# Kernel tuning notes

Measured on AMD Instinct MI355X. Metric: run time of the kernel, lower is better.

The kernel has to match this reference:

```python
import jax, jax.numpy as jnp
import numpy as np

B, T, S, D, H, FF = 4, 1024, 1024, 1024, 16, 4096
DH = D // H
NEG = -1e9
EPS = 1e-5


def setup_inputs() -> dict:
    key = jax.random.key(0)
    ks = jax.random.split(key, 20)
    p = 0.02  # param init scale
    inp = {
        "x": jax.random.normal(ks[0], (B, T, D), jnp.float32),
        "encoder_output": jax.random.normal(ks[1], (B, S, D), jnp.float32),
        "src_mask": jnp.ones((B, 1, 1, S), jnp.bool_),
        "tgt_mask": jnp.tril(jnp.ones((1, 1, T, T), jnp.bool_)),  # causal
        # self-attention params
        "d_Wq": jax.random.normal(ks[2], (D, D)) * p, "d_bq": jnp.zeros((D,)),
        "d_Wk": jax.random.normal(ks[3], (D, D)) * p, "d_bk": jnp.zeros((D,)),
        "d_Wv": jax.random.normal(ks[4], (D, D)) * p, "d_bv": jnp.zeros((D,)),
        "d_Wo": jax.random.normal(ks[5], (D, D)) * p, "d_bo": jnp.zeros((D,)),
        # cross-attention params
        "e_Wq": jax.random.normal(ks[6], (D, D)) * p, "e_bq": jnp.zeros((D,)),
        "e_Wk": jax.random.normal(ks[7], (D, D)) * p, "e_bk": jnp.zeros((D,)),
        "e_Wv": jax.random.normal(ks[8], (D, D)) * p, "e_bv": jnp.zeros((D,)),
        "e_Wo": jax.random.normal(ks[9], (D, D)) * p, "e_bo": jnp.zeros((D,)),
        # FFN params
        "ff_W1": jax.random.normal(ks[10], (D, FF)) * p, "ff_b1": jnp.zeros((FF,)),
        "ff_W2": jax.random.normal(ks[11], (FF, D)) * p, "ff_b2": jnp.zeros((D,)),
        # layernorm params
        "ln1_g": jnp.ones((D,)), "ln1_b": jnp.zeros((D,)),
        "ln2_g": jnp.ones((D,)), "ln2_b": jnp.zeros((D,)),
        "ln3_g": jnp.ones((D,)), "ln3_b": jnp.zeros((D,)),
    }
    return inp


def _mha(xq, xkv, Wq, bq, Wk, bk, Wv, bv, Wo, bo, mask):
    b, tq = xq.shape[0], xq.shape[1]
    q = (xq @ Wq + bq).reshape(b, tq, H, DH).transpose(0, 2, 1, 3)
    k = (xkv @ Wk + bk).reshape(b, -1, H, DH).transpose(0, 2, 1, 3)
    v = (xkv @ Wv + bv).reshape(b, -1, H, DH).transpose(0, 2, 1, 3)
    scores = jnp.einsum("bhqd,bhkd->bhqk", q, k) / np.float32(np.sqrt(DH))
    scores = jnp.where(mask, scores, NEG)
    attn = jax.nn.softmax(scores, axis=-1)
    out = jnp.einsum("bhqk,bhkd->bhqd", attn, v)
    out = out.transpose(0, 2, 1, 3).reshape(b, tq, D)
    return out @ Wo + bo


def _ln(x, g, b):
    m = jnp.mean(x, axis=-1, keepdims=True)
    v = jnp.var(x, axis=-1, keepdims=True)
    return (x - m) / jnp.sqrt(v + EPS) * g + b


def reference(x, encoder_output, src_mask, tgt_mask,
              d_Wq, d_bq, d_Wk, d_bk, d_Wv, d_bv, d_Wo, d_bo,
              e_Wq, e_bq, e_Wk, e_bk, e_Wv, e_bv, e_Wo, e_bo,
              ff_W1, ff_b1, ff_W2, ff_b2,
              ln1_g, ln1_b, ln2_g, ln2_b, ln3_g, ln3_b):
    # masked self-attention + residual + LN (dropout is identity in eval)
    d = _mha(x, x, d_Wq, d_bq, d_Wk, d_bk, d_Wv, d_bv, d_Wo, d_bo, tgt_mask)
    d = _ln(d + x, ln1_g, ln1_b)
    # cross-attention over encoder output + residual + LN
    f = _mha(d, encoder_output, e_Wq, e_bq, e_Wk, e_bk, e_Wv, e_bv, e_Wo, e_bo, src_mask)
    f = _ln(f + d, ln2_g, ln2_b)
    # FFN + residual + LN
    g = jax.nn.relu(f @ ff_W1 + ff_b1) @ ff_W2 + ff_b2
    g = _ln(g + f, ln3_g, ln3_b)
    return g
```

## Files before the change

kernel.cpp:

```cpp
#include <hip/hip_runtime.h>

static constexpr int Bc = 4, Tc = 1024, Sc = 1024, Dc = 1024, Hc = 16, DHc = 64, FFc = 4096;

typedef __attribute__((ext_vector_type(8))) short short8;
typedef __attribute__((ext_vector_type(4))) short short4v;
typedef __attribute__((ext_vector_type(4))) float f32x4;

struct P8 { unsigned short* o[8]; };

__device__ __forceinline__ unsigned short f2bf(float f) {
    unsigned int u = __float_as_uint(f);
    unsigned int r = u + 0x7fffu + ((u >> 16) & 1u);
    return (unsigned short)(r >> 16);
}
__device__ __forceinline__ float bf2f(unsigned short u) {
    return __uint_as_float(((unsigned int)u) << 16);
}
__device__ __forceinline__ float fexp2(float x) {
    float r; asm("v_exp_f32 %0, %1" : "=v"(r) : "v"(x)); return r;
}
__device__ __forceinline__ unsigned int cvtpk(float a, float b) {
    unsigned int r;
    asm("v_cvt_pk_bf16_f32 %0, %1, %2" : "=v"(r) : "v"(a), "v"(b));
    return r;
}

__device__ __forceinline__ void gload_lds16(const void* g, void* l) {
    __builtin_amdgcn_global_load_lds((const __attribute__((address_space(1))) void*)g,
                                     (__attribute__((address_space(3))) void*)l, 16, 0, 0);
}

__global__ __launch_bounds__(256) void cast2_f32_bf16(const float* __restrict__ inA,
                                                      const float* __restrict__ inB,
                                                      unsigned short* __restrict__ outA,
                                                      unsigned short* __restrict__ outB, int n8) {
    int i = blockIdx.x * 256 + threadIdx.x;
    if (i >= n8) return;
    const float* in = blockIdx.y ? inB : inA;
    unsigned short* out = blockIdx.y ? outB : outA;
    const float4* p = (const float4*)in + (size_t)i * 2;
    float4 a = p[0], b = p[1];
    short8 o;
    o[0] = f2bf(a.x); o[1] = f2bf(a.y); o[2] = f2bf(a.z); o[3] = f2bf(a.w);
    o[4] = f2bf(b.x); o[5] = f2bf(b.y); o[6] = f2bf(b.z); o[7] = f2bf(b.w);
    *(short8*)(out + (size_t)i * 8) = o;
}

struct TJ { const float* s; unsigned short* d; int ss, ds; float scl; };
struct TJ16 { TJ j[16]; };
__global__ __launch_bounds__(256) void transpose_cast16(TJ16 p) {
    __shared__ float t[64][65];
    const TJ jb = p.j[blockIdx.z];
    const int c0 = blockIdx.x * 64, r0 = blockIdx.y * 64;
    const int tid = threadIdx.x;
    const int rr = tid >> 2, cc = (tid & 3) * 16;
    const float* src = jb.s + (size_t)(r0 + rr) * jb.ss + c0 + cc;
#pragma unroll
    for (int i = 0; i < 4; i++) {
        float4 v = *(const float4*)(src + i * 4);
        t[rr][cc + i * 4 + 0] = v.x;
        t[rr][cc + i * 4 + 1] = v.y;
        t[rr][cc + i * 4 + 2] = v.z;
        t[rr][cc + i * 4 + 3] = v.w;
    }
    __syncthreads();
#pragma unroll
    for (int half = 0; half < 2; half++) {
        const int id = half * 256 + tid;
        const int a = id >> 3, b0 = id & 7;
        short8 o;
#pragma unroll
        for (int e = 0; e < 8; e++) o[e] = f2bf(t[b0 * 8 + e][a] * jb.scl);
        *(short8*)(jb.d + (size_t)(c0 + a) * jb.ds + r0 + b0 * 8) = o;
    }
}

__global__ void prep_bias(const float* dbq, const float* dbk, const float* dbv,
                          const float* ebk, const float* ebv, const float* ebq,
                          float* __restrict__ bqkv, float* __restrict__ bekv,
                          float* __restrict__ ebq_s, float SC) {
    int i = blockIdx.x * 256 + threadIdx.x;
    int seg = i >> 10, j = i & 1023;
    switch (seg) {
        case 0: bqkv[j] = dbq[j] * SC; break;
        case 1: bqkv[1024 + j] = dbk[j]; break;
        case 2: bqkv[2048 + j] = dbv[j]; break;
        case 3: bekv[j] = ebk[j]; break;
        case 4: bekv[1024 + j] = ebv[j]; break;
        default: ebq_s[j] = ebq[j] * SC; break;
    }
}

struct BlkMap { int m, n, z; };
__device__ __forceinline__ BlkMap remap_block() {
    const int gx = gridDim.x, gy = gridDim.y;
    const int nxy = gx * gy;
    const int nwg = nxy * gridDim.z;
    const int flat = (blockIdx.z * gy + blockIdx.y) * gx + blockIdx.x;
    const int id = (flat & 7) * (nwg >> 3) + (flat >> 3);
    const int pz = id / nxy;
    const int rz = id - pz * nxy;
    const int gwsh = (gx & 7) ? 2 : 3;
    const int gw = 1 << gwsh;
    const int gsz = gw * gy;
    const int grp = rz / gsz;
    const int rem = rz - grp * gsz;
    BlkMap r;
    r.m = rem >> gwsh;
    r.n = (grp << gwsh) + (rem & (gw - 1));
    r.z = pz;
    return r;
}

#define G256_BODY()                                                                            \
    stB(0, 0, 0); stA(0, 0, 0); stB(0, 1, 0); stA(0, 1, 0);                                    \
    stB(1, 0, 64); stA(1, 0, 64); stB(1, 1, 64);                                               \
    asm volatile("s_waitcnt vmcnt(6)" ::: "memory");                                           \
    __builtin_amdgcn_s_barrier();                                                              \
    const int nIter = nk >> 1;                                                                 \
    for (int it = 0; it < nIter; ++it) {                                                       \
        const int t_ = 2 * it, u_ = t_ + 1;                                                    \
        const int ku = u_ * 64;                                                                \
        const int kv = ((t_ + 2 < nk) ? t_ + 2 : t_) * 64;                                     \
        const int kw = ((u_ + 2 < nk) ? u_ + 2 : u_) * 64;                                     \
        ldB(0, 0, b0); ldA(0, 0, aF, aH);                                                      \
        stA(1, 1, ku);                                                                         \
        asm volatile("s_waitcnt lgkmcnt(8)" ::: "memory");                                     \
        __builtin_amdgcn_s_barrier();                                                          \
        asm volatile("s_waitcnt lgkmcnt(0)" ::: "memory");                                     \
        __builtin_amdgcn_s_setprio(1); MFMA16(aF, b0, 0); __builtin_amdgcn_s_setprio(0);       \
        __builtin_amdgcn_s_barrier();                                                          \
        ldB(0, 1, b1);                                                                         \
        stB(0, 0, kv);                                                                         \
        __builtin_amdgcn_s_barrier();                                                          \
        asm volatile("s_waitcnt lgkmcnt(0)" ::: "memory");                                     \
        __builtin_amdgcn_s_setprio(1); MFMA16(aH, b1, 0); __builtin_amdgcn_s_setprio(0);       \
        __builtin_amdgcn_s_barrier();                                                          \
        ldA(0, 1, aF, aH);                                                                     \
        stA(0, 0, kv);                                                                         \
        __builtin_amdgcn_s_barrier();                                                          \
        asm volatile("s_waitcnt lgkmcnt(0)" ::: "memory");                                     \
        __builtin_amdgcn_s_setprio(1); MFMA16(aH, b1, 4); __builtin_amdgcn_s_setprio(0);       \
        __builtin_amdgcn_s_barrier();                                                          \
        stB(0, 1, kv);                                                                         \
        __builtin_amdgcn_s_barrier();                                                          \
        __builtin_amdgcn_s_setprio(1); MFMA16(aF, b0, 4); __builtin_amdgcn_s_setprio(0);       \
        asm volatile("s_waitcnt vmcnt(6)" ::: "memory");                                       \
        __builtin_amdgcn_s_barrier();                                                          \
        ldB(1, 0, b0); ldA(1, 0, aF, aH);                                                      \
        stA(0, 1, kv);                                                                         \
        asm volatile("s_waitcnt lgkmcnt(8)" ::: "memory");                                     \
        __builtin_amdgcn_s_barrier();                                                          \
        asm volatile("s_waitcnt lgkmcnt(0)" ::: "memory");                                     \
        __builtin_amdgcn_s_setprio(1); MFMA16(aF, b0, 0); __builtin_amdgcn_s_setprio(0);       \
        __builtin_amdgcn_s_barrier();                                                          \
        ldB(1, 1, b1);                                                                         \
        stB(1, 0, kw);                                                                         \
        __builtin_amdgcn_s_barrier();                                                          \
        asm volatile("s_waitcnt lgkmcnt(0)" ::: "memory");                                     \
        __builtin_amdgcn_s_setprio(1); MFMA16(aH, b1, 0); __builtin_amdgcn_s_setprio(0);       \
        __builtin_amdgcn_s_barrier();                                                          \
        ldA(1, 1, aF, aH);                                                                     \
        stA(1, 0, kw);                                                                         \
        __builtin_amdgcn_s_barrier();                                                          \
        asm volatile("s_waitcnt lgkmcnt(0)" ::: "memory");                                     \
        __builtin_amdgcn_s_setprio(1); MFMA16(aH, b1, 4); __builtin_amdgcn_s_setprio(0);       \
        __builtin_amdgcn_s_barrier();                                                          \
        stB(1, 1, kw);                                                                         \
        __builtin_amdgcn_s_barrier();                                                          \
        __builtin_amdgcn_s_setprio(1); MFMA16(aF, b0, 4); __builtin_amdgcn_s_setprio(0);       \
        asm volatile("s_waitcnt vmcnt(6)" ::: "memory");                                       \
        __builtin_amdgcn_s_barrier();                                                          \
    }                                                                                          \
    asm volatile("s_waitcnt vmcnt(0)" ::: "memory");                                           \
    __syncthreads();

#define MFMA16(aa, bb, base)                                                                   \
    _Pragma("unroll") for (int m_ = 0; m_ < 4; m_++)                                           \
        _Pragma("unroll") for (int n_ = 0; n_ < 4; n_++)                                       \
            acc[(base) + m_][n_] = __builtin_amdgcn_mfma_f32_16x16x32_bf16(                    \
                (aa)[m_], (bb)[n_], acc[(base) + m_][n_], 0, 0, 0);

template <int EPI>
__global__ __launch_bounds__(512, 2) void gemm256(const unsigned short* __restrict__ A,
                                                  const unsigned short* __restrict__ Bt,
                                                  const float* __restrict__ bias,
                                                  unsigned short* __restrict__ outB,
                                                  int N, int lda, int ldb, int nk, P8 po) {
    __shared__ unsigned short SM[2][2][2][8192];
    const int tid = threadIdx.x;
    const int lane = tid & 63, wid = tid >> 6;
    const int l4 = lane & 15, g = lane >> 4;
    const int wr = wid >> 2, wc = wid & 3;
    BlkMap bm = remap_block();
    const int m0 = bm.m * 256, n0 = bm.n * 256, z = bm.z;
    A += (size_t)z * (nk * 64);
    Bt += (size_t)z * (nk * 64);
    const int sw = l4 & 7;

    const int fl0 = tid, fl1 = 512 + tid;
    const int lr0 = fl0 >> 3, ch0 = (fl0 & 7) ^ (lr0 & 7);
    const int lr1 = fl1 >> 3, ch1 = (fl1 & 7) ^ (lr1 & 7);
    const size_t A64 = (size_t)64 * lda;
    const unsigned short* pA0 = A + (size_t)(m0 + (lr0 >> 6) * 128 + (lr0 & 63)) * lda + ch0 * 8;
    const unsigned short* pA1 = A + (size_t)(m0 + (lr1 >> 6) * 128 + (lr1 & 63)) * lda + ch1 * 8;
    const unsigned short* pB0 = Bt + (size_t)(n0 + (ch0 >> 2) * 128 + lr0) * ldb + (ch0 & 3) * 8;
    const unsigned short* pB1 = Bt + (size_t)(n0 + (ch1 >> 2) * 128 + lr1) * ldb + (ch1 & 3) * 8;

    auto stA = [&](int d, int mh, int kofs) {
        char* base = (char*)&SM[0][d][mh][0];
        gload_lds16(pA0 + (size_t)mh * A64 + kofs, base + fl0 * 16);
        gload_lds16(pA1 + (size_t)mh * A64 + kofs, base + fl1 * 16);
    };
    auto stB = [&](int d, int ks, int kofs) {
        char* base = (char*)&SM[1][d][ks][0];
        gload_lds16(pB0 + ks * 32 + kofs, base + fl0 * 16);
        gload_lds16(pB1 + ks * 32 + kofs, base + fl1 * 16);
    };

    f32x4 acc[8][4] = {};
    short8 aF[4], aH[4], b0[4], b1[4];

    auto ldA = [&](int d, int mh, short8* d0, short8* d1) {
#pragma unroll
        for (int m = 0; m < 4; m++) {
            const char* rp = (const char*)&SM[0][d][mh][0] + (wr * 64 + m * 16 + l4) * 128;
            d0[m] = *(const short8*)(rp + ((g ^ sw) * 16));
            d1[m] = *(const short8*)(rp + (((4 + g) ^ sw) * 16));
        }
    };
    auto ldB = [&](int d, int ks, short8* dst) {
#pragma unroll
        for (int n = 0; n < 4; n++) {
            const char* rp = (const char*)&SM[1][d][ks][0] + ((wc & 1) * 64 + n * 16 + l4) * 128;
            dst[n] = *(const short8*)(rp + ((((wc >> 1) * 4 + g) ^ sw) * 16));
        }
    };

    G256_BODY()

    unsigned short* eb = (unsigned short*)SM;
    unsigned short* oB = (EPI == 3) ? po.o[z] : outB;
    const int colL = wc * 64 + l4;
#pragma unroll
    for (int h = 0; h < 2; ++h) {
        if (wr == h) {
#pragma unroll
            for (int mm = 0; mm < 8; mm++) {
                const int base_r = (mm < 4 ? mm * 16 : 64 + (mm - 4) * 16) + g * 4;
#pragma unroll
                for (int n = 0; n < 4; n++) {
                    float bv = (EPI == 3 && z != 0) ? 0.f : bias[n0 + colL + n * 16];
#pragma unroll
                    for (int r = 0; r < 4; r++) {
                        float v = acc[mm][n][r] + bv;
                        if (EPI == 2) v = fmaxf(v, 0.f);
                        eb[(base_r + r) * 260 + colL + n * 16] = f2bf(v);
                    }
                }
            }
        }
        __syncthreads();
        const int gr0 = m0 + h * 128;
#pragma unroll
        for (int j = 0; j < 8; j++) {
            const int f = j * 8192 + tid * 16;
            const int row = f >> 9;
            const int colb = f & 511;
            short8 v = *(const short8*)((const char*)eb + row * 520 + colb);
            *(short8*)(oB + (size_t)(gr0 + row) * N + n0 + (colb >> 1)) = v;
        }
        if (h == 0) __syncthreads();
    }
}

struct GJob {
    const unsigned short *A, *Bt;
    const float* bias;
    unsigned short *out, *vt;
    int N, lda, ldb, nk, vthresh, nwg, gx;
};
struct GJ2 { GJob j[2]; };
__global__ __launch_bounds__(512, 2) void gemm256j(GJ2 p) {
    __shared__ unsigned short SM[2][2][2][8192];
    const int tid = threadIdx.x;
    const int lane = tid & 63, wid = tid >> 6;
    const int l4 = lane & 15, g = lane >> 4;
    const int wr = wid >> 2, wc = wid & 3;

    int f = blockIdx.x;
    const int ji = (f < p.j[0].nwg) ? 0 : 1;
    if (ji) f -= p.j[0].nwg;
    const GJob jb = p.j[ji];
    const int id = (f & 7) * (jb.nwg >> 3) + (f >> 3);
    const int gwsh = (jb.gx & 7) ? 2 : 3;
    const int gw = 1 << gwsh;
    const int gy = jb.nwg / jb.gx;
    const int gsz = gw * gy;
    const int grp = id / gsz;
    const int rem = id - grp * gsz;
    const int m0 = (rem >> gwsh) * 256;
    const int n0 = ((grp << gwsh) + (rem & (gw - 1))) * 256;

    const unsigned short* A = jb.A;
    const unsigned short* Bt = jb.Bt;
    const int lda = jb.lda, ldb = jb.ldb, nk = jb.nk;
    const int sw = l4 & 7;

    const int fl0 = tid, fl1 = 512 + tid;
    const int lr0 = fl0 >> 3, ch0 = (fl0 & 7) ^ (lr0 & 7);
    const int lr1 = fl1 >> 3, ch1 = (fl1 & 7) ^ (lr1 & 7);
    const size_t A64 = (size_t)64 * lda;
    const unsigned short* pA0 = A + (size_t)(m0 + (lr0 >> 6) * 128 + (lr0 & 63)) * lda + ch0 * 8;
    const unsigned short* pA1 = A + (size_t)(m0 + (lr1 >> 6) * 128 + (lr1 & 63)) * lda + ch1 * 8;
    const unsigned short* pB0 = Bt + (size_t)(n0 + (ch0 >> 2) * 128 + lr0) * ldb + (ch0 & 3) * 8;
    const unsigned short* pB1 = Bt + (size_t)(n0 + (ch1 >> 2) * 128 + lr1) * ldb + (ch1 & 3) * 8;

    auto stA = [&](int d, int mh, int kofs) {
        char* base = (char*)&SM[0][d][mh][0];
        gload_lds16(pA0 + (size_t)mh * A64 + kofs, base + fl0 * 16);
        gload_lds16(pA1 + (size_t)mh * A64 + kofs, base + fl1 * 16);
    };
    auto stB = [&](int d, int ks, int kofs) {
        char* base = (char*)&SM[1][d][ks][0];
        gload_lds16(pB0 + ks * 32 + kofs, base + fl0 * 16);
        gload_lds16(pB1 + ks * 32 + kofs, base + fl1 * 16);
    };

    f32x4 acc[8][4] = {};
    short8 aF[4], aH[4], b0[4], b1[4];

    auto ldA = [&](int d, int mh, short8* d0, short8* d1) {
#pragma unroll
        for (int m = 0; m < 4; m++) {
            const char* rp = (const char*)&SM[0][d][mh][0] + (wr * 64 + m * 16 + l4) * 128;
            d0[m] = *(const short8*)(rp + ((g ^ sw) * 16));
            d1[m] = *(const short8*)(rp + (((4 + g) ^ sw) * 16));
        }
    };
    auto ldB = [&](int d, int ks, short8* dst) {
#pragma unroll
        for (int n = 0; n < 4; n++) {
            const char* rp = (const char*)&SM[1][d][ks][0] + ((wc & 1) * 64 + n * 16 + l4) * 128;
            dst[n] = *(const short8*)(rp + ((((wc >> 1) * 4 + g) ^ sw) * 16));
        }
    };

    G256_BODY()

    unsigned short* eb = (unsigned short*)SM;
    const int colL = wc * 64 + l4;
#pragma unroll
    for (int h = 0; h < 2; ++h) {
        if (wr == h) {
#pragma unroll
            for (int mm = 0; mm < 8; mm++) {
                const int base_r = (mm < 4 ? mm * 16 : 64 + (mm - 4) * 16) + g * 4;
#pragma unroll
                for (int n = 0; n < 4; n++) {
                    float bv = jb.bias[n0 + colL + n * 16];
#pragma unroll
                    for (int r = 0; r < 4; r++)
                        eb[(base_r + r) * 260 + colL + n * 16] = f2bf(acc[mm][n][r] + bv);
                }
            }
        }
        __syncthreads();
        const int gr0 = m0 + h * 128;
        if (n0 >= jb.vthresh) {
            const int b_ = gr0 >> 10, sb = gr0 & 1023;
#pragma unroll
            for (int j = 0; j < 4; j++) {
                const int id2 = j * 512 + tid;
                const int col = id2 & 255, rseg = id2 >> 8;
                const int rel = n0 - jb.vthresh + col;
                const int hh = rel >> 6, dh = rel & 63;
                short8 v0, v1;
#pragma unroll
                for (int e = 0; e < 8; e++) {
                    v0[e] = eb[(rseg * 16 + e) * 260 + col];
                    v1[e] = eb[(rseg * 16 + 8 + e) * 260 + col];
                }
                unsigned short* dp = jb.vt +
                    ((size_t)(b_ * 16 + hh) * 64 + dh) * 1024 + sb + rseg * 16;
                *(short8*)dp = v0;
                *(short8*)(dp + 8) = v1;
            }
        } else {
#pragma unroll
            for (int j = 0; j < 8; j++) {
                const int ff = j * 8192 + tid * 16;
                const int row = ff >> 9;
                const int colb = ff & 511;
                short8 v = *(const short8*)((const char*)eb + row * 520 + colb);
                *(short8*)(jb.out + (size_t)(gr0 + row) * jb.N + n0 + (colb >> 1)) = v;
            }
        }
        if (h == 0) __syncthreads();
    }
}

template <int EPI>
__global__ __launch_bounds__(256) void gemm64_db(const unsigned short* __restrict__ A,
                                                 const unsigned short* __restrict__ Bt,
                                                 const float* __restrict__ bias,
                                                 float* __restrict__ outF,
                                                 unsigned short* __restrict__ outB,
                                                 int M, int N, int Kloop, int lda, int ldb) {
    __shared__ unsigned short As[3][64 * 32];
    __shared__ unsigned short Bs[3][128 * 32];
    const int tid = threadIdx.x;
    const int w = tid >> 6, lane = tid & 63, l4 = lane & 15, g = lane >> 4;
    BlkMap bm = remap_block();
    const int m0 = bm.m * 64, n0 = bm.n * 128;
    f32x4 acc[4][2] = {};
    const int r0 = tid >> 2;
    const int kk = ((tid & 3) ^ ((tid >> 3) & 3)) * 8;
    const int sk = (l4 >> 1) & 3;
    const unsigned short* Ar0 = A + (size_t)(m0 + r0) * lda + kk;
    const unsigned short* Br0 = Bt + (size_t)(n0 + r0) * ldb + kk;
    const unsigned short* Br1 = Bt + (size_t)(n0 + 64 + r0) * ldb + kk;
    auto stage = [&](int sb, int k0) {
        gload_lds16(Ar0 + k0, (char*)As[sb] + tid * 16);
        gload_lds16(Br0 + k0, (char*)Bs[sb] + tid * 16);
        gload_lds16(Br1 + k0, (char*)Bs[sb] + 4096 + tid * 16);
    };
    const int nk = Kloop >> 5;
    stage(0, 0);
    stage(1, 32);
    asm volatile("s_waitcnt vmcnt(3)" ::: "memory");
    __builtin_amdgcn_s_barrier();
    asm volatile("" ::: "memory");
    int buf = 0;
    for (int t = 0; t < nk; ++t) {
        if (t + 2 < nk) {
            int b2 = buf + 2; if (b2 >= 3) b2 -= 3;
            stage(b2, (t + 2) * 32);
        }
        short8 a[4], b[2];
#pragma unroll
        for (int m = 0; m < 4; m++)
            a[m] = *(const short8*)(As[buf] + (m * 16 + l4) * 32 + (g ^ sk) * 8);
#pragma unroll
        for (int n = 0; n < 2; n++)
            b[n] = *(const short8*)(Bs[buf] + (w * 32 + n * 16 + l4) * 32 + (g ^ sk) * 8);
#pragma unroll
        for (int m = 0; m < 4; m++)
#pragma unroll
            for (int n = 0; n < 2; n++)
                acc[m][n] = __builtin_amdgcn_mfma_f32_16x16x32_bf16(a[m], b[n], acc[m][n], 0, 0, 0);
        if (t + 1 < nk) {
            if (t + 2 < nk) asm volatile("s_waitcnt vmcnt(3)" ::: "memory");
            else            asm volatile("s_waitcnt vmcnt(0)" ::: "memory");
            __builtin_amdgcn_s_barrier();
            asm volatile("" ::: "memory");
        }
        buf = (buf + 1 == 3) ? 0 : buf + 1;
    }
    const int rowB = m0 + g * 4;
    const int colB = n0 + w * 32 + l4;
#pragma unroll
    for (int n = 0; n < 2; n++) {
        float bv = bias[colB + n * 16];
#pragma unroll
        for (int m = 0; m < 4; m++) {
#pragma unroll
            for (int r = 0; r < 4; r++) {
                float v = acc[m][n][r] + bv;
                if (EPI == 2) v = fmaxf(v, 0.f);
                size_t idx = (size_t)(rowB + m * 16 + r) * N + colB + n * 16;
                if (EPI == 1) outF[idx] = v;
                else outB[idx] = f2bf(v);
            }
        }
    }
}

template <int CAUSAL>
__global__ __launch_bounds__(512) void attn6_kernel(const unsigned short* __restrict__ Q, int ldq,
                                                    const unsigned short* __restrict__ Kg, int ldk,
                                                    const unsigned short* __restrict__ Vt,
                                                    unsigned short* __restrict__ O) {
    __shared__ unsigned short Kl[2 * 64 * 64];
    __shared__ unsigned short Vl[2 * 64 * 64];
    __shared__ unsigned short Pl[8][16 * 72];
    const int bh = blockIdx.x;
    const int qb = CAUSAL ? (gridDim.y - 1 - blockIdx.y) : blockIdx.y;
    const int b = bh >> 4, h = bh & 15;
    const int tid = threadIdx.x, w = tid >> 6, lane = tid & 63;
    const int l4 = lane & 15, g = lane >> 4;
    const int q0 = qb * 128 + w * 16;
    const unsigned short* Qp = Q + (size_t)(b * Tc + q0 + l4) * ldq + h * DHc + g * 8;
    short8 qf0 = *(const short8*)Qp;
    short8 qf1 = *(const short8*)(Qp + 32);
    const unsigned short* Kbase = Kg + (size_t)(b * 1024) * ldk + h * DHc;
    const unsigned short* Vbase = Vt + (size_t)bh * DHc * 1024;
    f32x4 o[4] = {};
    float mrun = -1e30f, lrun = 0.f;
    const int nT = CAUSAL ? 2 * qb + 2 : 16;
    unsigned short* pw = &Pl[w][l4 * 72];
    const int qi = q0 + l4;

    short8 ones;
#pragma unroll
    for (int j = 0; j < 8; j++) ones[j] = (short)0x3F80;

    const int sr = tid >> 3;
    const int sc_ = (tid & 7) ^ (sr & 7);

    auto stage = [&](int s0, int buf) {
        char* kd = (char*)Kl + buf * 8192;
        char* vd = (char*)Vl + buf * 8192;
        gload_lds16(Kbase + (size_t)(s0 + sr) * ldk + sc_ * 8, kd + tid * 16);
        gload_lds16(Vbase + (size_t)sr * 1024 + s0 + sc_ * 8, vd + tid * 16);
    };

    stage(0, 0);
    __syncthreads();
    int buf = 0;
    const int sw = l4 & 7;

    for (int t = 0; t < nT; ++t) {
        const int s0 = t * 64;
        if (t + 1 < nT) stage(s0 + 64, buf ^ 1);
        if (!CAUSAL || s0 <= q0 + 15) {
            const unsigned short* Kb_ = Kl + buf * 4096;
            const unsigned short* Vb_ = Vl + buf * 4096;
            f32x4 st[4];
            f32x4 z = {0.f, 0.f, 0.f, 0.f};
            __builtin_amdgcn_s_setprio(1);
#pragma unroll
            for (int c = 0; c < 4; c++) {
                const unsigned short* kr = Kb_ + (c * 16 + l4) * 64;
                short8 ka0 = *(const short8*)(kr + ((g ^ sw) * 8));
                short8 ka1 = *(const short8*)(kr + (((g + 4) ^ sw) * 8));
                st[c] = __builtin_amdgcn_mfma_f32_16x16x32_bf16(ka0, qf0, z, 0, 0, 0);
                st[c] = __builtin_amdgcn_mfma_f32_16x16x32_bf16(ka1, qf1, st[c], 0, 0, 0);
            }
            __builtin_amdgcn_s_setprio(0);
            float p[16];
            const bool domask = CAUSAL && (s0 + 63 > q0);
#pragma unroll
            for (int c = 0; c < 4; c++)
#pragma unroll
                for (int r = 0; r < 4; r++) {
                    float v = st[c][r];
                    if (domask && (s0 + c * 16 + g * 4 + r) > qi) v = -1e9f;
                    p[c * 4 + r] = v;
                }
            float m1 = fmaxf(fmaxf(p[0], p[1]), p[2]);
            float m2 = fmaxf(fmaxf(p[3], p[4]), p[5]);
            float m3 = fmaxf(fmaxf(p[6], p[7]), p[8]);
            float m4 = fmaxf(fmaxf(p[9], p[10]), p[11]);
            float m5 = fmaxf(fmaxf(p[12], p[13]), p[14]);
            float tmax = fmaxf(fmaxf(fmaxf(m1, m2), fmaxf(m3, m4)), fmaxf(m5, p[15]));
            tmax = fmaxf(tmax, __shfl_xor(tmax, 16));
            tmax = fmaxf(tmax, __shfl_xor(tmax, 32));
            if (!__all(tmax <= mrun + 11.5f)) {
                float mnew = fmaxf(mrun, tmax);
                float al = fexp2(mrun - mnew);
                lrun *= al;
#pragma unroll
                for (int d = 0; d < 4; d++) o[d] *= al;
                mrun = mnew;
            }
#pragma unroll
            for (int i = 0; i < 16; i++) p[i] = fexp2(p[i] - mrun);
#pragma unroll
            for (int c = 0; c < 4; c++) {
                uint2 u;
                u.x = cvtpk(p[c * 4 + 0], p[c * 4 + 1]);
                u.y = cvtpk(p[c * 4 + 2], p[c * 4 + 3]);
                *(uint2*)(pw + c * 16 + g * 4) = u;
            }
            short8 pb_lo = *(const short8*)(pw + g * 8);
            short8 pb_hi = *(const short8*)(pw + 32 + g * 8);
            __builtin_amdgcn_s_setprio(1);
            f32x4 s4 = __builtin_amdgcn_mfma_f32_16x16x32_bf16(ones, pb_lo, z, 0, 0, 0);
            s4 = __builtin_amdgcn_mfma_f32_16x16x32_bf16(ones, pb_hi, s4, 0, 0, 0);
#pragma unroll
            for (int d = 0; d < 4; d++) {
                const unsigned short* vr = Vb_ + (d * 16 + l4) * 64;
                short8 va0 = *(const short8*)(vr + ((g ^ sw) * 8));
                short8 va1 = *(const short8*)(vr + (((g + 4) ^ sw) * 8));
                o[d] = __builtin_amdgcn_mfma_f32_16x16x32_bf16(va0, pb_lo, o[d], 0, 0, 0);
                o[d] = __builtin_amdgcn_mfma_f32_16x16x32_bf16(va1, pb_hi, o[d], 0, 0, 0);
            }
            __builtin_amdgcn_s_setprio(0);
            lrun += s4[0];
        }
        __syncthreads();
        buf ^= 1;
    }
    float inv = 1.f / lrun;
    unsigned short* Ob = O + (size_t)(b * Tc + q0 + l4) * Dc + h * DHc;
#pragma unroll
    for (int d = 0; d < 4; d++) {
#pragma unroll
        for (int r = 0; r < 4; r++) Ob[d * 16 + g * 4 + r] = f2bf(o[d][r] * inv);
    }
}

__global__ __launch_bounds__(256) void ln_bf(const unsigned short* __restrict__ a,
                                             const unsigned short* __restrict__ res,
                                             const float* __restrict__ gam,
                                             const float* __restrict__ bet,
                                             unsigned short* __restrict__ outB,
                                             float* __restrict__ outF) {
    int row = blockIdx.x, t = threadIdx.x;
    size_t base = (size_t)row * Dc + t * 4;
    short4v av = *(const short4v*)(a + base);
    short4v rv = *(const short4v*)(res + base);
    float x0 = bf2f((unsigned short)av[0]) + bf2f((unsigned short)rv[0]);
    float x1 = bf2f((unsigned short)av[1]) + bf2f((unsigned short)rv[1]);
    float x2 = bf2f((unsigned short)av[2]) + bf2f((unsigned short)rv[2]);
    float x3 = bf2f((unsigned short)av[3]) + bf2f((unsigned short)rv[3]);
    float s = x0 + x1 + x2 + x3;
    float ss = x0 * x0 + x1 * x1 + x2 * x2 + x3 * x3;
    for (int o = 1; o < 64; o <<= 1) { s += __shfl_xor(s, o); ss += __shfl_xor(ss, o); }
    __shared__ float S1[4], S2[4];
    int w = t >> 6;
    if ((t & 63) == 0) { S1[w] = s; S2[w] = ss; }
    __syncthreads();
    s = S1[0] + S1[1] + S1[2] + S1[3];
    ss = S2[0] + S2[1] + S2[2] + S2[3];
    float mean = s * (1.f / Dc);
    float var = ss * (1.f / Dc) - mean * mean;
    float rstd = rsqrtf(var + 1e-5f);
    int c = t * 4;
    float4 g4 = *(const float4*)(gam + c);
    float4 b4 = *(const float4*)(bet + c);
    float y0 = (x0 - mean) * rstd * g4.x + b4.x;
    float y1 = (x1 - mean) * rstd * g4.y + b4.y;
    float y2 = (x2 - mean) * rstd * g4.z + b4.z;
    float y3 = (x3 - mean) * rstd * g4.w + b4.w;
    if (outB) {
        short4v ob;
        ob[0] = f2bf(y0); ob[1] = f2bf(y1); ob[2] = f2bf(y2); ob[3] = f2bf(y3);
        *(short4v*)(outB + base) = ob;
    }
    if (outF) { float4 ov = {y0, y1, y2, y3}; *(float4*)(outF + base) = ov; }
}

__global__ __launch_bounds__(256) void ln_4b(const unsigned short* __restrict__ p,
                                             const unsigned short* __restrict__ res,
                                             const float* __restrict__ gam,
                                             const float* __restrict__ bet,
                                             float* __restrict__ outF) {
    const size_t PS = (size_t)4096 * 1024;
    int row = blockIdx.x, t = threadIdx.x;
    size_t base = (size_t)row * Dc + t * 4;
    float x0, x1, x2, x3;
    {
        short4v rv = *(const short4v*)(res + base);
        x0 = bf2f((unsigned short)rv[0]); x1 = bf2f((unsigned short)rv[1]);
        x2 = bf2f((unsigned short)rv[2]); x3 = bf2f((unsigned short)rv[3]);
    }
#pragma unroll
    for (int j = 0; j < 4; j++) {
        short4v v = *(const short4v*)(p + j * PS + base);
        x0 += bf2f((unsigned short)v[0]); x1 += bf2f((unsigned short)v[1]);
        x2 += bf2f((unsigned short)v[2]); x3 += bf2f((unsigned short)v[3]);
    }
    float s = x0 + x1 + x2 + x3;
    float ss = x0 * x0 + x1 * x1 + x2 * x2 + x3 * x3;
    for (int o = 1; o < 64; o <<= 1) { s += __shfl_xor(s, o); ss += __shfl_xor(ss, o); }
    __shared__ float S1[4], S2[4];
    int w = t >> 6;
    if ((t & 63) == 0) { S1[w] = s; S2[w] = ss; }
    __syncthreads();
    s = S1[0] + S1[1] + S1[2] + S1[3];
    ss = S2[0] + S2[1] + S2[2] + S2[3];
    float mean = s * (1.f / Dc);
    float var = ss * (1.f / Dc) - mean * mean;
    float rstd = rsqrtf(var + 1e-5f);
    int c = t * 4;
    float4 g4 = *(const float4*)(gam + c);
    float4 b4 = *(const float4*)(bet + c);
    float4 ov;
    ov.x = (x0 - mean) * rstd * g4.x + b4.x;
    ov.y = (x1 - mean) * rstd * g4.y + b4.y;
    ov.z = (x2 - mean) * rstd * g4.z + b4.z;
    ov.w = (x3 - mean) * rstd * g4.w + b4.w;
    *(float4*)(outF + base) = ov;
}

extern "C" void kernel_launch(void* const* d_in, const int* in_sizes, int n_in,
                              void* d_out, int out_size, void* d_ws, size_t ws_size,
                              hipStream_t stream) {
    const float* x   = (const float*)d_in[0];
    const float* enc = (const float*)d_in[1];
    const float* dWq = (const float*)d_in[4];  const float* dbq = (const float*)d_in[5];
    const float* dWk = (const float*)d_in[6];  const float* dbk = (const float*)d_in[7];
    const float* dWv = (const float*)d_in[8];  const float* dbv = (const float*)d_in[9];
    const float* dWo = (const float*)d_in[10]; const float* dbo = (const float*)d_in[11];
    const float* eWq = (const float*)d_in[12]; const float* ebq = (const float*)d_in[13];
    const float* eWk = (const float*)d_in[14]; const float* ebk = (const float*)d_in[15];
    const float* eWv = (const float*)d_in[16]; const float* ebv = (const float*)d_in[17];
    const float* eWo = (const float*)d_in[18]; const float* ebo = (const float*)d_in[19];
    const float* fW1 = (const float*)d_in[20]; const float* fb1 = (const float*)d_in[21];
    const float* fW2 = (const float*)d_in[22]; const float* fb2 = (const float*)d_in[23];
    const float* g1 = (const float*)d_in[24];  const float* be1 = (const float*)d_in[25];
    const float* g2 = (const float*)d_in[26];  const float* be2 = (const float*)d_in[27];
    const float* g3 = (const float*)d_in[28];  const float* be3 = (const float*)d_in[29];

    const float SC = 0.125f * 1.44269504f;

    char* ws = (char*)d_ws;
    size_t off = 0;
    auto alloc = [&](size_t bytes) -> void* {
        void* p = ws + off;
        off += (bytes + 255) & ~(size_t)255;
        return p;
    };
    const size_t A = (size_t)4096 * 1024;
    const size_t MB1 = (size_t)1024 * 1024;
    char* R1 = (char*)alloc(32 * 1024 * 1024);
    unsigned short* qkv = (unsigned short*)R1;
    unsigned short* qx  = (unsigned short*)(R1 + 16 * 1024 * 1024);
    unsigned short* h1  = (unsigned short*)R1;
    unsigned short* xb   = (unsigned short*)alloc(A * 2);
    unsigned short* encb = (unsigned short*)alloc(A * 2);
    unsigned short* wqkv = (unsigned short*)alloc(3 * MB1 * 2);
    unsigned short* wekv = (unsigned short*)alloc(2 * MB1 * 2);
    unsigned short* weq  = (unsigned short*)alloc(MB1 * 2);
    unsigned short* wdo  = (unsigned short*)alloc(MB1 * 2);
    unsigned short* weo  = (unsigned short*)alloc(MB1 * 2);
    unsigned short* wf1  = (unsigned short*)alloc(4 * MB1 * 2);
    unsigned short* wf2  = (unsigned short*)alloc(4 * MB1 * 2);
    float* bqkv = (float*)alloc(3072 * 4);
    float* bekv = (float*)alloc(2048 * 4);
    float* ebq_s = (float*)alloc(1024 * 4);
    unsigned short* VtB = (unsigned short*)alloc(A * 2);
    unsigned short* ab  = (unsigned short*)alloc(A * 2);
    unsigned short* tmpB = (unsigned short*)alloc(A * 2);
    unsigned short* dB = (unsigned short*)alloc(A * 2);
    unsigned short* fB = (unsigned short*)alloc(A * 2);
    unsigned short* kb  = (unsigned short*)alloc(A * 2);
    unsigned short* vtc = (unsigned short*)alloc(A * 2);
    unsigned short* pfb = VtB;
    (void)ws_size; (void)in_sizes; (void)n_in; (void)out_size;

    cast2_f32_bf16<<<dim3(2048, 2), 256, 0, stream>>>(x, enc, xb, encb, (int)(A / 8));

    TJ16 tj;
    tj.j[0] = {dWq, wqkv,           1024, 1024, SC};
    tj.j[1] = {dWk, wqkv + MB1,     1024, 1024, 1.f};
    tj.j[2] = {dWv, wqkv + 2 * MB1, 1024, 1024, 1.f};
    tj.j[3] = {eWk, wekv,           1024, 1024, 1.f};
    tj.j[4] = {eWv, wekv + MB1,     1024, 1024, 1.f};
    tj.j[5] = {eWq, weq,            1024, 1024, SC};
    tj.j[6] = {dWo, wdo,            1024, 1024, 1.f};
    tj.j[7] = {eWo, weo,            1024, 1024, 1.f};
    for (int jj = 0; jj < 4; jj++) {
        tj.j[8 + jj]  = {fW1 + 1024 * jj, wf1 + (size_t)1024 * jj * 1024, 4096, 1024, 1.f};
        tj.j[12 + jj] = {fW2 + (size_t)1024 * jj * 1024, wf2 + 1024 * jj, 1024, 4096, 1.f};
    }
    transpose_cast16<<<dim3(16, 16, 16), 256, 0, stream>>>(tj);
    prep_bias<<<24, 256, 0, stream>>>(dbq, dbk, dbv, ebk, ebv, ebq, bqkv, bekv, ebq_s, SC);

    P8 z8{};

    {
        GJ2 gj;
        gj.j[0] = {xb, wqkv, bqkv, qkv, VtB, 3072, 1024, 1024, 16, 2048, 192, 12};
        gj.j[1] = {encb, wekv, bekv, kb, vtc, 1024, 1024, 1024, 16, 1024, 128, 8};
        gemm256j<<<dim3(320), 512, 0, stream>>>(gj);
    }

    attn6_kernel<1><<<dim3(64, 8), 512, 0, stream>>>(qkv, 3072, qkv + 1024, 3072, VtB, ab);
    gemm64_db<0><<<dim3(8, 64), 256, 0, stream>>>(ab, wdo, dbo, nullptr, tmpB, 4096, 1024, 1024, 1024, 1024);
    ln_bf<<<4096, 256, 0, stream>>>(tmpB, xb, g1, be1, dB, nullptr);

    gemm64_db<0><<<dim3(8, 64), 256, 0, stream>>>(dB, weq, ebq_s, nullptr, qx, 4096, 1024, 1024, 1024, 1024);
    attn6_kernel<0><<<dim3(64, 8), 512, 0, stream>>>(qx, 1024, kb, 1024, vtc, ab);
    gemm64_db<0><<<dim3(8, 64), 256, 0, stream>>>(ab, weo, ebo, nullptr, tmpB, 4096, 1024, 1024, 1024, 1024);
    ln_bf<<<4096, 256, 0, stream>>>(tmpB, dB, g2, be2, fB, nullptr);

    gemm256<2><<<dim3(16, 16), 512, 0, stream>>>(fB, wf1, fb1, h1, 4096, 1024, 1024, 16, z8);
    {
        P8 pf{};
        pf.o[0] = pfb;
        pf.o[1] = pfb + A;
        pf.o[2] = pfb + 2 * A;
        pf.o[3] = pfb + 3 * A;
        gemm256<3><<<dim3(4, 16, 4), 512, 0, stream>>>(h1, wf2, fb2, nullptr, 1024, 4096, 4096, 16, pf);
    }
    ln_4b<<<4096, 256, 0, stream>>>(pfb, fB, g3, be3, (float*)d_out);
}
```

Before: 313.8 us.

## Replace 256x256 FFN GEMM with 128x256 tile kernel and simpler double buffering

Swaps the 256x256-tile gemm256 kernel used for both FFN GEMMs for a new 128x256-tile kernel with K-step 32 and a plain two-stage LDS double buffer, launched with 4 blocks per CU. This doubles the block count (512 instead of 256 for FF1) to improve CU occupancy and wave balance on the many-CU device. The cost is lower arithmetic intensity per tile, more global reloads of the B operand, and more barrier iterations per K.

```diff
diff --git a/kernel.cpp b/kernel.cpp
--- a/kernel.cpp
+++ b/kernel.cpp
@@ -181,99 +181,6 @@
             acc[(base) + m_][n_] = __builtin_amdgcn_mfma_f32_16x16x32_bf16(                    \
                 (aa)[m_], (bb)[n_], acc[(base) + m_][n_], 0, 0, 0);
 
-template <int EPI>
-__global__ __launch_bounds__(512, 2) void gemm256(const unsigned short* __restrict__ A,
-                                                  const unsigned short* __restrict__ Bt,
-                                                  const float* __restrict__ bias,
-                                                  unsigned short* __restrict__ outB,
-                                                  int N, int lda, int ldb, int nk, P8 po) {
-    __shared__ unsigned short SM[2][2][2][8192];
-    const int tid = threadIdx.x;
-    const int lane = tid & 63, wid = tid >> 6;
-    const int l4 = lane & 15, g = lane >> 4;
-    const int wr = wid >> 2, wc = wid & 3;
-    BlkMap bm = remap_block();
-    const int m0 = bm.m * 256, n0 = bm.n * 256, z = bm.z;
-    A += (size_t)z * (nk * 64);
-    Bt += (size_t)z * (nk * 64);
-    const int sw = l4 & 7;
-
-    const int fl0 = tid, fl1 = 512 + tid;
-    const int lr0 = fl0 >> 3, ch0 = (fl0 & 7) ^ (lr0 & 7);
-    const int lr1 = fl1 >> 3, ch1 = (fl1 & 7) ^ (lr1 & 7);
-    const size_t A64 = (size_t)64 * lda;
-    const unsigned short* pA0 = A + (size_t)(m0 + (lr0 >> 6) * 128 + (lr0 & 63)) * lda + ch0 * 8;
-    const unsigned short* pA1 = A + (size_t)(m0 + (lr1 >> 6) * 128 + (lr1 & 63)) * lda + ch1 * 8;
-    const unsigned short* pB0 = Bt + (size_t)(n0 + (ch0 >> 2) * 128 + lr0) * ldb + (ch0 & 3) * 8;
-    const unsigned short* pB1 = Bt + (size_t)(n0 + (ch1 >> 2) * 128 + lr1) * ldb + (ch1 & 3) * 8;
-
-    auto stA = [&](int d, int mh, int kofs) {
-        char* base = (char*)&SM[0][d][mh][0];
-        gload_lds16(pA0 + (size_t)mh * A64 + kofs, base + fl0 * 16);
-        gload_lds16(pA1 + (size_t)mh * A64 + kofs, base + fl1 * 16);
-    };
-    auto stB = [&](int d, int ks, int kofs) {
-        char* base = (char*)&SM[1][d][ks][0];
-        gload_lds16(pB0 + ks * 32 + kofs, base + fl0 * 16);
-        gload_lds16(pB1 + ks * 32 + kofs, base + fl1 * 16);
-    };
-
-    f32x4 acc[8][4] = {};
-    short8 aF[4], aH[4], b0[4], b1[4];
-
-    auto ldA = [&](int d, int mh, short8* d0, short8* d1) {
-#pragma unroll
-        for (int m = 0; m < 4; m++) {
-            const char* rp = (const char*)&SM[0][d][mh][0] + (wr * 64 + m * 16 + l4) * 128;
-            d0[m] = *(const short8*)(rp + ((g ^ sw) * 16));
-            d1[m] = *(const short8*)(rp + (((4 + g) ^ sw) * 16));
-        }
-    };
-    auto ldB = [&](int d, int ks, short8* dst) {
-#pragma unroll
-        for (int n = 0; n < 4; n++) {
-            const char* rp = (const char*)&SM[1][d][ks][0] + ((wc & 1) * 64 + n * 16 + l4) * 128;
-            dst[n] = *(const short8*)(rp + ((((wc >> 1) * 4 + g) ^ sw) * 16));
-        }
-    };
-
-    G256_BODY()
-
-    unsigned short* eb = (unsigned short*)SM;
-    unsigned short* oB = (EPI == 3) ? po.o[z] : outB;
-    const int colL = wc * 64 + l4;
-#pragma unroll
-    for (int h = 0; h < 2; ++h) {
-        if (wr == h) {
-#pragma unroll
-            for (int mm = 0; mm < 8; mm++) {
-                const int base_r = (mm < 4 ? mm * 16 : 64 + (mm - 4) * 16) + g * 4;
-#pragma unroll
-                for (int n = 0; n < 4; n++) {
-                    float bv = (EPI == 3 && z != 0) ? 0.f : bias[n0 + colL + n * 16];
-#pragma unroll
-                    for (int r = 0; r < 4; r++) {
-                        float v = acc[mm][n][r] + bv;
-                        if (EPI == 2) v = fmaxf(v, 0.f);
-                        eb[(base_r + r) * 260 + colL + n * 16] = f2bf(v);
-                    }
-                }
-            }
-        }
-        __syncthreads();
-        const int gr0 = m0 + h * 128;
-#pragma unroll
-        for (int j = 0; j < 8; j++) {
-            const int f = j * 8192 + tid * 16;
-            const int row = f >> 9;
-            const int colb = f & 511;
-            short8 v = *(const short8*)((const char*)eb + row * 520 + colb);
-            *(short8*)(oB + (size_t)(gr0 + row) * N + n0 + (colb >> 1)) = v;
-        }
-        if (h == 0) __syncthreads();
-    }
-}
-
 struct GJob {
     const unsigned short *A, *Bt;
     const float* bias;
@@ -395,6 +302,113 @@
                 short8 v = *(const short8*)((const char*)eb + row * 520 + colb);
                 *(short8*)(jb.out + (size_t)(gr0 + row) * jb.N + n0 + (colb >> 1)) = v;
             }
+        }
+        if (h == 0) __syncthreads();
+    }
+}
+
+template <int EPI>
+__global__ __launch_bounds__(512, 4) void gemm128x256(const unsigned short* __restrict__ A,
+                                                      const unsigned short* __restrict__ Bt,
+                                                      const float* __restrict__ bias,
+                                                      unsigned short* __restrict__ outB,
+                                                      int N, int lda, int ldb, int nk, P8 po) {
+    __shared__ unsigned short SMEM[24576];
+    unsigned short* As0 = SMEM;
+    unsigned short* As1 = SMEM + 4096;
+    unsigned short* Bs0 = SMEM + 8192;
+    unsigned short* Bs1 = SMEM + 16384;
+    const int tid = threadIdx.x;
+    const int lane = tid & 63, wid = tid >> 6;
+    const int l4 = lane & 15, g = lane >> 4;
+    const int wr = wid >> 2, wc = wid & 3;
+    BlkMap bm = remap_block();
+    const int m0 = bm.m * 128, n0 = bm.n * 256, z = bm.z;
+    A += (size_t)z * (nk * 32);
+    Bt += (size_t)z * (nk * 32);
+
+    const int ra = tid >> 2, ca = (tid & 3) ^ (ra & 3);
+    const int sb1 = 512 + tid;
+    const int rb0 = tid >> 2, cb0 = (tid & 3) ^ (rb0 & 3);
+    const int rb1 = sb1 >> 2, cb1 = (sb1 & 3) ^ (rb1 & 3);
+    const unsigned short* pA = A + (size_t)(m0 + ra) * lda + ca * 8;
+    const unsigned short* pB0 = Bt + (size_t)(n0 + rb0) * ldb + cb0 * 8;
+    const unsigned short* pB1 = Bt + (size_t)(n0 + rb1) * ldb + cb1 * 8;
+    auto stage = [&](int d, int kofs) {
+        gload_lds16(pA + kofs, (char*)(d ? As1 : As0) + tid * 16);
+        gload_lds16(pB0 + kofs, (char*)(d ? Bs1 : Bs0) + tid * 16);
+        gload_lds16(pB1 + kofs, (char*)(d ? Bs1 : Bs0) + sb1 * 16);
+    };
+
+    f32x4 acc[4][4] = {};
+    stage(0, 0);
+    if (nk > 1) stage(1, 32);
+    asm volatile("s_waitcnt vmcnt(3)" ::: "memory");
+    __builtin_amdgcn_s_barrier();
+
+    for (int t = 0; t < nk; ++t) {
+        const int cur = t & 1;
+        const unsigned short* Asr = cur ? As1 : As0;
+        const unsigned short* Bsr = cur ? Bs1 : Bs0;
+        short8 a[4], b[4];
+#pragma unroll
+        for (int m = 0; m < 4; m++) {
+            const int row = wr * 64 + m * 16 + l4;
+            a[m] = *(const short8*)(Asr + row * 32 + ((g ^ (row & 3)) * 8));
+        }
+#pragma unroll
+        for (int n = 0; n < 4; n++) {
+            const int row = wc * 64 + n * 16 + l4;
+            b[n] = *(const short8*)(Bsr + row * 32 + ((g ^ (row & 3)) * 8));
+        }
+        asm volatile("s_waitcnt lgkmcnt(0)" ::: "memory");
+        __builtin_amdgcn_sched_barrier(0);
+        __builtin_amdgcn_s_barrier();
+        if (t + 2 < nk) stage(cur, (t + 2) * 32);
+        __builtin_amdgcn_s_setprio(1);
+#pragma unroll
+        for (int m = 0; m < 4; m++)
+#pragma unroll
+            for (int n = 0; n < 4; n++)
+                acc[m][n] = __builtin_amdgcn_mfma_f32_16x16x32_bf16(a[m], b[n], acc[m][n], 0, 0, 0);
+        __builtin_amdgcn_s_setprio(0);
+        if (t + 1 < nk) {
+            if (t + 2 < nk) asm volatile("s_waitcnt vmcnt(3)" ::: "memory");
+            else            asm volatile("s_waitcnt vmcnt(0)" ::: "memory");
+            __builtin_amdgcn_s_barrier();
+        }
+    }
+    __syncthreads();
+
+    unsigned short* eb = SMEM;
+    unsigned short* oB = (EPI == 3) ? po.o[z] : outB;
+    const int colL = wc * 64 + l4;
+#pragma unroll
+    for (int h = 0; h < 2; ++h) {
+        if (wr == h) {
+#pragma unroll
+            for (int mm = 0; mm < 4; mm++) {
+                const int lr = mm * 16 + g * 4;
+#pragma unroll
+                for (int n = 0; n < 4; n++) {
+                    float bv = (EPI == 3 && z != 0) ? 0.f : bias[n0 + colL + n * 16];
+#pragma unroll
+                    for (int r = 0; r < 4; r++) {
+                        float v = acc[mm][n][r] + bv;
+                        if (EPI == 2) v = fmaxf(v, 0.f);
+                        eb[(lr + r) * 260 + colL + n * 16] = f2bf(v);
+                    }
+                }
+            }
+        }
+        __syncthreads();
+        const int gr0 = m0 + h * 64;
+#pragma unroll
+        for (int j = 0; j < 4; j++) {
+            const int id2 = j * 512 + tid;
+            const int row = id2 >> 5, c8 = (id2 & 31) * 8;
+            short8 v = *(const short8*)(eb + row * 260 + c8);
+            *(short8*)(oB + (size_t)(gr0 + row) * N + n0 + c8) = v;
         }
         if (h == 0) __syncthreads();
     }
@@ -777,14 +791,14 @@
     gemm64_db<0><<<dim3(8, 64), 256, 0, stream>>>(ab, weo, ebo, nullptr, tmpB, 4096, 1024, 1024, 1024, 1024);
     ln_bf<<<4096, 256, 0, stream>>>(tmpB, dB, g2, be2, fB, nullptr);
 
-    gemm256<2><<<dim3(16, 16), 512, 0, stream>>>(fB, wf1, fb1, h1, 4096, 1024, 1024, 16, z8);
+    gemm128x256<2><<<dim3(16, 32), 512, 0, stream>>>(fB, wf1, fb1, h1, 4096, 1024, 1024, 32, z8);
     {
         P8 pf{};
         pf.o[0] = pfb;
         pf.o[1] = pfb + A;
         pf.o[2] = pfb + 2 * A;
         pf.o[3] = pfb + 3 * A;
-        gemm256<3><<<dim3(4, 16, 4), 512, 0, stream>>>(h1, wf2, fb2, nullptr, 1024, 4096, 4096, 16, pf);
+        gemm128x256<3><<<dim3(4, 32, 4), 512, 0, stream>>>(h1, wf2, fb2, nullptr, 1024, 4096, 4096, 32, pf);
     }
     ln_4b<<<4096, 256, 0, stream>>>(pfb, fB, g3, be3, (float*)d_out);
 }
```

Result: no change. 317.8 us (+1.3%).
